# Kernel tuning notes

Measured on AMD Instinct MI355X. Metric: run time of the kernel, lower is better.

The kernel has to match this reference:

```python
import jax, jax.numpy as jnp
import numpy as np

B, N, C, H, AD, HID = 2, 1024, 768, 12, 8, 3072
SCALE = (C // H) ** -0.5


def setup_inputs() -> dict:
    key = jax.random.key(0)
    ks = jax.random.split(key, 32)
    inp = {}
    for i in range(5):
        inp[f"x{i}"] = jax.random.normal(ks[i], (B, N, C), jnp.float32)
    def w(i, shape, s=0.02):
        return jax.random.normal(ks[i], shape, jnp.float32) * s
    inp.update({
        "ln1_g": jnp.ones((C,), jnp.float32), "ln1_b": jnp.zeros((C,), jnp.float32),
        "ln2_g": jnp.ones((C,), jnp.float32), "ln2_b": jnp.zeros((C,), jnp.float32),
        "qkv_w": w(5, (C, 3 * C)), "qkv_b": jnp.zeros((3 * C,), jnp.float32),
        "proj_w": w(6, (C, C)), "proj_b": jnp.zeros((C,), jnp.float32),
        "fc1_w": w(7, (C, HID)), "fc1_b": jnp.zeros((HID,), jnp.float32),
        "fc2_w": w(8, (HID, C)), "fc2_b": jnp.zeros((C,), jnp.float32),
        "at_dw": w(9, (C, AD)), "at_db": jnp.zeros((AD,), jnp.float32),
        "at_mw": w(10, (AD, AD)), "at_mb": jnp.zeros((AD,), jnp.float32),
        "at_uw": w(11, (AD, C)), "at_ub": jnp.zeros((C,), jnp.float32),
        "a2_dw": w(12, (C, AD)), "a2_db": jnp.zeros((AD,), jnp.float32),
        "a2_mw": w(13, (AD, AD)), "a2_mb": jnp.zeros((AD,), jnp.float32),
        "a2_uw": w(14, (AD, C)), "a2_ub": jnp.zeros((C,), jnp.float32),
    })
    return inp


def _ln(x, g, b, eps=1e-5):
    mu = x.mean(-1, keepdims=True)
    xc = x - mu
    var = (xc * xc).mean(-1, keepdims=True)
    return xc * jax.lax.rsqrt(var + eps) * g + b


def _adapter(x, dw, db, mw, mb, uw, ub):
    h = x @ dw + db          # bottleneck down [., AD]
    h = h @ mw + mb          # mid
    return h @ uw + ub       # up back to C


def _attn(x, qkv_w, qkv_b, proj_w, proj_b):
    # x: [S, B, N, C] (streams folded in leading axis)
    s, b, n, c = x.shape
    qkv = (x @ qkv_w + qkv_b).reshape(s, b, n, 3, H, c // H)
    q, k, v = jnp.moveaxis(qkv, 3, 0)            # each [S,B,N,H,D]
    scores = jnp.einsum('sbnhd,sbmhd->sbhnm', q * SCALE, k)  # fp32; clamp is a no-op
    p = jax.nn.softmax(scores, axis=-1)
    o = jnp.einsum('sbhnm,sbmhd->sbnhd', p, v).reshape(s, b, n, c)
    return o @ proj_w + proj_b


def reference(x0, x1, x2, x3, x4,
              ln1_g, ln1_b, ln2_g, ln2_b,
              qkv_w, qkv_b, proj_w, proj_b,
              fc1_w, fc1_b, fc2_w, fc2_b,
              at_dw, at_db, at_mw, at_mb, at_uw, at_ub,
              a2_dw, a2_db, a2_mw, a2_mb, a2_uw, a2_ub):
    xs = jnp.stack([x0, x1, x2, x3, x4])          # [5,B,N,C]
    n1 = _ln(xs, ln1_g, ln1_b)
    a1 = _adapter(n1, at_dw, at_db, at_mw, at_mb, at_uw, at_ub)
    ao = _attn(n1, qkv_w, qkv_b, proj_w, proj_b)
    # cross-stream residuals: x01=a1[0], x12=a1[1], ..., x10=a1[1], x21=a1[2], ...
    y0 = xs[0] + ao[0] + a1[1]
    y1 = xs[1] + ao[1] + a1[0] + a1[2]
    y2 = xs[2] + ao[2] + a1[1] + a1[3]
    y3 = xs[3] + ao[3] + a1[2] + a1[4]
    y4 = xs[4] + ao[4] + a1[3]
    ys = jnp.stack([y0, y1, y2, y3, y4])
    a2 = _adapter(_ln(ys, ln1_g, ln1_b), a2_dw, a2_db, a2_mw, a2_mb, a2_uw, a2_ub)
    h = _ln(ys, ln2_g, ln2_b) @ fc1_w + fc1_b
    m = jax.nn.gelu(h, approximate=False) @ fc2_w + fc2_b
    z0 = ys[0] + m[0] + a2[1]
    z1 = ys[1] + m[1] + a2[0] + a2[2]
    z2 = ys[2] + m[2] + a2[1] + a2[3]
    z3 = ys[3] + m[3] + a2[2] + a2[4]
    z4 = ys[4] + m[4] + a2[3]
    return jnp.stack([z0, z1, z2, z3, z4])        # [5,B,N,C]
```

## Files before the change

kernel.cpp:

```cpp
#include <hip/hip_runtime.h>
#include <math.h>

typedef __bf16 bf16;
typedef __attribute__((ext_vector_type(8))) __bf16 bf16x8;
typedef __attribute__((ext_vector_type(4))) __bf16 bf16x4;
typedef __attribute__((ext_vector_type(4))) float f32x4;
typedef __attribute__((ext_vector_type(16))) float f32x16;

#define TOK   10240
#define CD    768
#define NQKV  2304
#define NHID  3072
#define SEQ   1024
#define NH    12

__device__ __forceinline__ f32x4 mfma16(bf16x8 a, bf16x8 b, f32x4 c) {
  return __builtin_amdgcn_mfma_f32_16x16x32_bf16(a, b, c, 0, 0, 0);
}
__device__ __forceinline__ f32x16 mfma32(bf16x8 a, bf16x8 b, f32x16 c) {
  return __builtin_amdgcn_mfma_f32_32x32x16_bf16(a, b, c, 0, 0, 0);
}

__device__ __forceinline__ void gload16(const void* g, void* l) {
  __builtin_amdgcn_global_load_lds(
      (const __attribute__((address_space(1))) void*)g,
      (__attribute__((address_space(3))) void*)l, 16, 0, 0);
}

__device__ __forceinline__ unsigned pack2(bf16 a, bf16 b) {
  union { unsigned short u[2]; unsigned v; } x;
  x.u[0] = __builtin_bit_cast(unsigned short, a);
  x.u[1] = __builtin_bit_cast(unsigned short, b);
  return x.v;
}

__device__ __forceinline__ f32x4 b4tof(const bf16* p) {
  bf16x4 v = *(const bf16x4*)p;
  f32x4 r;
#pragma unroll
  for (int j = 0; j < 4; ++j) r[j] = (float)v[j];
  return r;
}

__device__ __forceinline__ float fast_gelu(float v) {
  float u = 0.7978845608f * (v + 0.044715f * v * v * v);
  float e = __expf(fminf(2.f * u, 30.f));
  return 0.5f * v * (1.f + (e - 1.f) / (e + 1.f));
}

__global__ __launch_bounds__(256) void transpose_to_bf16(
    const float* __restrict__ in, bf16* __restrict__ out, int K, int N) {
  __shared__ float tile[32][33];
  const int bn = blockIdx.x * 32, bk = blockIdx.y * 32;
  const int r = threadIdx.x >> 5, c = threadIdx.x & 31;
#pragma unroll
  for (int i = 0; i < 4; ++i)
    tile[r + 8 * i][c] = in[(size_t)(bk + r + 8 * i) * N + bn + c];
  __syncthreads();
#pragma unroll
  for (int i = 0; i < 4; ++i)
    out[(size_t)(bn + r + 8 * i) * K + bk + c] = (bf16)tile[c][r + 8 * i];
}

__global__ __launch_bounds__(256) void ln5_kernel(
    const float* __restrict__ x0, const float* __restrict__ x1,
    const float* __restrict__ x2, const float* __restrict__ x3,
    const float* __restrict__ x4, const float* __restrict__ g,
    const float* __restrict__ b, bf16* __restrict__ out) {
  const int w = threadIdx.x >> 6, lane = threadIdx.x & 63;
  const int row = blockIdx.x * 4 + w;
  const int s = row >> 11, rem = row & 2047;
  const float* xp;
  switch (s) {
    case 0: xp = x0; break; case 1: xp = x1; break; case 2: xp = x2; break;
    case 3: xp = x3; break; default: xp = x4; break;
  }
  const f32x4* xr = (const f32x4*)(xp + (size_t)rem * CD);
  f32x4 v[3];
#pragma unroll
  for (int i = 0; i < 3; ++i) v[i] = xr[lane + 64 * i];
  float sum = 0.f;
#pragma unroll
  for (int i = 0; i < 3; ++i)
#pragma unroll
    for (int j = 0; j < 4; ++j) sum += v[i][j];
#pragma unroll
  for (int m = 32; m >= 1; m >>= 1) sum += __shfl_xor(sum, m);
  const float mu = sum * (1.f / 768.f);
  float vs = 0.f;
#pragma unroll
  for (int i = 0; i < 3; ++i)
#pragma unroll
    for (int j = 0; j < 4; ++j) { float d = v[i][j] - mu; vs += d * d; }
#pragma unroll
  for (int m = 32; m >= 1; m >>= 1) vs += __shfl_xor(vs, m);
  const float rstd = rsqrtf(vs * (1.f / 768.f) + 1e-5f);
  const f32x4* gp = (const f32x4*)g;
  const f32x4* bp = (const f32x4*)b;
  bf16* orow = out + (size_t)row * CD;
#pragma unroll
  for (int i = 0; i < 3; ++i) {
    const int c4 = lane + 64 * i;
    f32x4 gg = gp[c4], bb = bp[c4];
    bf16x4 o;
#pragma unroll
    for (int j = 0; j < 4; ++j)
      o[j] = (bf16)((v[i][j] - mu) * rstd * gg[j] + bb[j]);
    *(bf16x4*)(orow + c4 * 4) = o;
  }
}

__global__ __launch_bounds__(256) void fuse_res_ln(
    const float* __restrict__ x0, const float* __restrict__ x1,
    const float* __restrict__ x2, const float* __restrict__ x3,
    const float* __restrict__ x4, const bf16* __restrict__ m01,
    const bf16* __restrict__ a, float* __restrict__ ys,
    const float* __restrict__ g1, const float* __restrict__ b1,
    const float* __restrict__ g2, const float* __restrict__ b2,
    bf16* __restrict__ o1, bf16* __restrict__ o2) {
  const int w = threadIdx.x >> 6, lane = threadIdx.x & 63;
  const int row = blockIdx.x * 4 + w;
  const int s = row >> 11, rem = row & 2047;
  const float* xp;
  switch (s) {
    case 0: xp = x0; break; case 1: xp = x1; break; case 2: xp = x2; break;
    case 3: xp = x3; break; default: xp = x4; break;
  }
  const f32x4* xr = (const f32x4*)(xp + (size_t)rem * CD);
  const bf16* p0 = m01 + (size_t)row * CD;
  const bf16* p1 = m01 + (size_t)TOK * CD + (size_t)row * CD;
  const bf16* am = a + (size_t)(row - 2048) * CD;
  const bf16* ap = a + (size_t)(row + 2048) * CD;
  f32x4 v[3];
#pragma unroll
  for (int i = 0; i < 3; ++i) {
    const int c4 = lane + 64 * i;
    f32x4 t = xr[c4] + b4tof(p0 + c4 * 4) + b4tof(p1 + c4 * 4);
    if (s > 0) t += b4tof(am + c4 * 4);
    if (s < 4) t += b4tof(ap + c4 * 4);
    v[i] = t;
  }
  f32x4* yr = (f32x4*)(ys + (size_t)row * CD);
#pragma unroll
  for (int i = 0; i < 3; ++i) yr[lane + 64 * i] = v[i];

  float sum = 0.f;
#pragma unroll
  for (int i = 0; i < 3; ++i)
#pragma unroll
    for (int j = 0; j < 4; ++j) sum += v[i][j];
#pragma unroll
  for (int m = 32; m >= 1; m >>= 1) sum += __shfl_xor(sum, m);
  const float mu = sum * (1.f / 768.f);
  float vs = 0.f;
#pragma unroll
  for (int i = 0; i < 3; ++i)
#pragma unroll
    for (int j = 0; j < 4; ++j) { float d = v[i][j] - mu; vs += d * d; }
#pragma unroll
  for (int m = 32; m >= 1; m >>= 1) vs += __shfl_xor(vs, m);
  const float rstd = rsqrtf(vs * (1.f / 768.f) + 1e-5f);
  bf16* r1 = o1 + (size_t)row * CD;
  bf16* r2 = o2 + (size_t)row * CD;
#pragma unroll
  for (int i = 0; i < 3; ++i) {
    const int c4 = lane + 64 * i;
    f32x4 gg1 = ((const f32x4*)g1)[c4], bb1 = ((const f32x4*)b1)[c4];
    f32x4 gg2 = ((const f32x4*)g2)[c4], bb2 = ((const f32x4*)b2)[c4];
    bf16x4 oa, ob;
#pragma unroll
    for (int j = 0; j < 4; ++j) {
      float n = (v[i][j] - mu) * rstd;
      oa[j] = (bf16)(n * gg1[j] + bb1[j]);
      ob[j] = (bf16)(n * gg2[j] + bb2[j]);
    }
    *(bf16x4*)(r1 + c4 * 4) = oa;
    *(bf16x4*)(r2 + c4 * 4) = ob;
  }
}

template <int EPI>
__global__ __launch_bounds__(512, 2) void gemm256(
    const bf16* __restrict__ A, const bf16* __restrict__ Bt,
    const float* __restrict__ bias, void* __restrict__ Cout, int N, int Klen,
    int ldk, int nbn, int bpk, size_t kpstride) {
  __shared__ bf16 As[2][8192];
  __shared__ bf16 Bs[2][8192];
  const int t = threadIdx.x, lane = t & 63, w = t >> 6;
  const int wm = w >> 2, wn = w & 3;

  const int chunkg = gridDim.x >> 3;
  const int wg = (blockIdx.x & 7) * chunkg + (blockIdx.x >> 3);
  const int kp = wg / bpk, rem = wg % bpk;
  const int bm = rem / nbn, bn = rem % nbn;

  f32x4 acc[8][4] = {};

  const int srow = t >> 2;
  const int scol = ((t & 3) ^ ((srow >> 1) & 3)) << 3;
  const size_t koff = (size_t)kp * Klen;
  const bf16* Ab = A + (size_t)(bm * 256 + srow) * ldk + koff + scol;
  const bf16* Bb = Bt + (size_t)(bn * 256 + srow) * ldk + koff + scol;
  const size_t r128 = (size_t)128 * ldk;

  auto stage = [&](int buf, int kt) {
    const bf16* ga = Ab + (size_t)kt * 32;
    const bf16* gb = Bb + (size_t)kt * 32;
    gload16(ga, &As[buf][w * 512]);
    gload16(ga + r128, &As[buf][4096 + w * 512]);
    gload16(gb, &Bs[buf][w * 512]);
    gload16(gb + r128, &Bs[buf][4096 + w * 512]);
  };

  const int arow = wm * 128 + (lane & 15);
  const int brow = wn * 64 + (lane & 15);
  const int achn = (((lane >> 4) ^ ((lane >> 1) & 3)) << 3);

  stage(0, 0);
  stage(1, 1);
  asm volatile("s_waitcnt vmcnt(4)" ::: "memory");
  __builtin_amdgcn_s_barrier();

  const int NT = Klen >> 5;
  bf16x8 af[8], bfr[4];

  for (int kt = 0; kt < NT; ++kt) {
    const int buf = kt & 1;
#pragma unroll
    for (int m_ = 0; m_ < 8; ++m_)
      af[m_] = *(const bf16x8*)&As[buf][(arow + m_ * 16) * 32 + achn];
#pragma unroll
    for (int n_ = 0; n_ < 4; ++n_)
      bfr[n_] = *(const bf16x8*)&Bs[buf][(brow + n_ * 16) * 32 + achn];
    asm volatile("s_waitcnt lgkmcnt(0)" ::: "memory");
    __builtin_amdgcn_s_barrier();
    if (kt + 2 < NT) {
      stage(buf, kt + 2);
      asm volatile("s_waitcnt vmcnt(4)" ::: "memory");
    } else {
      asm volatile("s_waitcnt vmcnt(0)" ::: "memory");
    }
    __builtin_amdgcn_s_barrier();
    __builtin_amdgcn_s_setprio(1);
#pragma unroll
    for (int m_ = 0; m_ < 8; ++m_)
#pragma unroll
      for (int n_ = 0; n_ < 4; ++n_)
        acc[m_][n_] = mfma16(af[m_], bfr[n_], acc[m_][n_]);
    __builtin_amdgcn_s_setprio(0);
  }

#pragma unroll
  for (int m_ = 0; m_ < 8; ++m_) {
    const int grow0 = bm * 256 + wm * 128 + m_ * 16 + (lane >> 4) * 4;
#pragma unroll
    for (int n_ = 0; n_ < 4; ++n_) {
      const int gcol = bn * 256 + wn * 64 + n_ * 16 + (lane & 15);
      const float bv = (kp == 0) ? bias[gcol] : 0.f;
#pragma unroll
      for (int r = 0; r < 4; ++r) {
        float v = acc[m_][n_][r] + bv;
        if (EPI == 2) v = fast_gelu(v);
        const size_t idx = (size_t)(grow0 + r) * N + gcol + kp * kpstride;
        if (EPI == 0) ((float*)Cout)[idx] = v;
        else ((bf16*)Cout)[idx] = (bf16)v;
      }
    }
  }
}

__global__ __launch_bounds__(256, 3) void attn_v2(
    const bf16* __restrict__ qkv, bf16* __restrict__ obuf) {
  __shared__ bf16 Ks[2][4096];
  __shared__ bf16 Vt[2][4096];
  const int t = threadIdx.x, lane = t & 63, w = t >> 6;
  const int g = lane >> 5, q32 = lane & 31, rq7 = q32 & 7;

  const int xcd = blockIdx.x & 7, slot = blockIdx.x >> 3;
  const int work = xcd * 120 + slot;
  const int sbh = work >> 3, qt = work & 7;
  const int sb = sbh / NH, h = sbh % NH;
  const size_t tokbase = (size_t)sb * SEQ;
  const int qoff = h * 64, koff = CD + h * 64, voff = 2 * CD + h * 64;

  const int qrow = qt * 128 + w * 32 + q32;
  bf16x8 qf[4];
  {
    const bf16* qp = qkv + (tokbase + qrow) * NQKV + qoff + g * 8;
#pragma unroll
    for (int kd = 0; kd < 4; ++kd) {
      bf16x8 v = *(const bf16x8*)(qp + kd * 16);
#pragma unroll
      for (int j = 0; j < 8; ++j) v[j] = (bf16)((float)v[j] * 0.125f);
      qf[kd] = v;
    }
  }

  const int skv1 = t >> 3, sc1 = (t & 7) ^ (skv1 & 7);
  const int skv2 = (t + 256) >> 3, sc2 = (t & 7) ^ (skv2 & 7);
  const int vkv0 = 2 * (t & 31);
  const int vd0 = 8 * (t >> 5);
  const int c0 = (vkv0 & 51) | ((vkv0 & 4) << 1) | ((vkv0 & 8) >> 1);
  const int vchunk = c0 >> 3, vsub = c0 & 7;
  const bf16* kbase = qkv + tokbase * NQKV + koff;
  const bf16* vbase = qkv + tokbase * NQKV + voff;

  {
    const bf16* kb0 = kbase;
    gload16(kb0 + (size_t)skv1 * NQKV + sc1 * 8, &Ks[0][w * 512]);
    gload16(kb0 + (size_t)skv2 * NQKV + sc2 * 8, &Ks[0][2048 + w * 512]);
    const bf16* vp = vbase + (size_t)vkv0 * NQKV + vd0;
    bf16x8 r0 = *(const bf16x8*)vp;
    bf16x8 r1 = *(const bf16x8*)(vp + NQKV);
#pragma unroll
    for (int j = 0; j < 8; ++j) {
      const int d = vd0 + j;
      *(unsigned*)&Vt[0][d * 64 + ((vchunk ^ j) << 3) + vsub] =
          pack2(r0[j], r1[j]);
    }
  }
  __syncthreads();

  float m_run = -1e30f, l_run = 0.f;
  f32x16 oT0 = {}, oT1 = {};
  int cur = 0;

  for (int kt = 0; kt < 16; ++kt) {
    bf16x8 nv0, nv1;
    if (kt < 15) {
      const bf16* vp = vbase + (size_t)((kt + 1) * 64 + vkv0) * NQKV + vd0;
      nv0 = *(const bf16x8*)vp;
      nv1 = *(const bf16x8*)(vp + NQKV);
      const bf16* kb0 = kbase + (size_t)(kt + 1) * 64 * NQKV;
      gload16(kb0 + (size_t)skv1 * NQKV + sc1 * 8, &Ks[cur ^ 1][w * 512]);
      gload16(kb0 + (size_t)skv2 * NQKV + sc2 * 8,
              &Ks[cur ^ 1][2048 + w * 512]);
    }

    f32x16 sT0 = {}, sT1 = {};
#pragma unroll
    for (int kd = 0; kd < 4; ++kd) {
      bf16x8 kf0 =
          *(const bf16x8*)&Ks[cur][q32 * 64 + (((2 * kd + g) ^ rq7) << 3)];
      bf16x8 kf1 = *(const bf16x8*)&Ks[cur][(32 + q32) * 64 +
                                            (((2 * kd + g) ^ rq7) << 3)];
      sT0 = mfma32(kf0, qf[kd], sT0);
      sT1 = mfma32(kf1, qf[kd], sT1);
    }

    float mt = sT0[0];
#pragma unroll
    for (int r = 1; r < 16; ++r) mt = fmaxf(mt, sT0[r]);
#pragma unroll
    for (int r = 0; r < 16; ++r) mt = fmaxf(mt, sT1[r]);
    mt = fmaxf(mt, __shfl_xor(mt, 32));
    const float mnew = fmaxf(m_run, mt);
    const float alpha = __expf(m_run - mnew);
    m_run = mnew;
    float rs = 0.f;
#pragma unroll
    for (int r = 0; r < 16; ++r) {
      sT0[r] = __expf(sT0[r] - mnew);
      rs += sT0[r];
    }
#pragma unroll
    for (int r = 0; r < 16; ++r) {
      sT1[r] = __expf(sT1[r] - mnew);
      rs += sT1[r];
    }
    rs += __shfl_xor(rs, 32);
    l_run = l_run * alpha + rs;
#pragma unroll
    for (int r = 0; r < 16; ++r) { oT0[r] *= alpha; oT1[r] *= alpha; }

    bf16x8 pa[4];
#pragma unroll
    for (int hh = 0; hh < 2; ++hh)
#pragma unroll
      for (int j = 0; j < 8; ++j) {
        pa[hh][j] = (bf16)sT0[8 * hh + j];
        pa[2 + hh][j] = (bf16)sT1[8 * hh + j];
      }

#pragma unroll
    for (int ks = 0; ks < 4; ++ks) {
      bf16x8 vf0 =
          *(const bf16x8*)&Vt[cur][q32 * 64 + (((2 * ks + g) ^ rq7) << 3)];
      bf16x8 vf1 = *(const bf16x8*)&Vt[cur][(32 + q32) * 64 +
                                            (((2 * ks + g) ^ rq7) << 3)];
      oT0 = mfma32(vf0, pa[ks], oT0);
      oT1 = mfma32(vf1, pa[ks], oT1);
    }

    if (kt < 15) {
#pragma unroll
      for (int j = 0; j < 8; ++j) {
        const int d = vd0 + j;
        *(unsigned*)&Vt[cur ^ 1][d * 64 + ((vchunk ^ j) << 3) + vsub] =
            pack2(nv0[j], nv1[j]);
      }
    }
    __syncthreads();
    cur ^= 1;
  }

  const float rl = 1.f / l_run;
  bf16* orow = obuf + (tokbase + qrow) * CD + h * 64;
#pragma unroll
  for (int m = 0; m < 4; ++m) {
    bf16x4 o0, o1;
#pragma unroll
    for (int r = 0; r < 4; ++r) {
      o0[r] = (bf16)(oT0[4 * m + r] * rl);
      o1[r] = (bf16)(oT1[4 * m + r] * rl);
    }
    *(bf16x4*)(orow + 8 * m + 4 * g) = o0;
    *(bf16x4*)(orow + 32 + 8 * m + 4 * g) = o1;
  }
}

__global__ __launch_bounds__(256) void adapter_kernel(
    const bf16* __restrict__ X, const float* __restrict__ dw,
    const float* __restrict__ db, const float* __restrict__ mw,
    const float* __restrict__ mb, const float* __restrict__ uw,
    const float* __restrict__ ub, bf16* __restrict__ out) {
  const int tok = blockIdx.x * 4 + (threadIdx.x >> 6);
  const int lane = threadIdx.x & 63;
  const bf16* xr = X + (size_t)tok * CD;
  float xv[12];
#pragma unroll
  for (int i = 0; i < 12; ++i) xv[i] = (float)xr[lane + 64 * i];
  float h1[8] = {0, 0, 0, 0, 0, 0, 0, 0};
#pragma unroll
  for (int i = 0; i < 12; ++i) {
    const f32x4* dr = (const f32x4*)(dw + (size_t)(lane + 64 * i) * 8);
    f32x4 d0 = dr[0], d1 = dr[1];
#pragma unroll
    for (int j = 0; j < 4; ++j) {
      h1[j] += xv[i] * d0[j];
      h1[4 + j] += xv[i] * d1[j];
    }
  }
#pragma unroll
  for (int m = 1; m < 64; m <<= 1)
#pragma unroll
    for (int j = 0; j < 8; ++j) h1[j] += __shfl_xor(h1[j], m);
#pragma unroll
  for (int j = 0; j < 8; ++j) h1[j] += db[j];
  float h2[8];
#pragma unroll
  for (int k = 0; k < 8; ++k) {
    float v = mb[k];
#pragma unroll
    for (int j = 0; j < 8; ++j) v += h1[j] * mw[j * 8 + k];
    h2[k] = v;
  }
#pragma unroll
  for (int i = 0; i < 12; ++i) {
    const int c = lane + 64 * i;
    float v = ub[c];
#pragma unroll
    for (int k = 0; k < 8; ++k) v += h2[k] * uw[k * CD + c];
    out[(size_t)tok * CD + c] = (bf16)v;
  }
}

__global__ __launch_bounds__(256) void cross_residual(
    const float* __restrict__ ys, const bf16* __restrict__ m01,
    const bf16* __restrict__ a, float* __restrict__ out) {
  const int s = blockIdx.y;
  const size_t i = (size_t)blockIdx.x * 256 + threadIdx.x;
  const size_t spitch = (size_t)2048 * 768 / 4;
  const size_t sb = (size_t)s * spitch;
  const size_t mstride = (size_t)TOK * CD / 4;
  f32x4 v = ((const f32x4*)ys)[sb + i];
  v += b4tof(m01 + (sb + i) * 4);
  v += b4tof(m01 + (mstride + sb + i) * 4);
  if (s > 0) v += b4tof(a + (sb - spitch + i) * 4);
  if (s < 4) v += b4tof(a + (sb + spitch + i) * 4);
  ((f32x4*)out)[sb + i] = v;
}

#define OFF_WTQKV  ((size_t)0)
#define OFF_WTPROJ ((size_t)3538944)
#define OFF_WTFC1  ((size_t)4718592)
#define OFF_WTFC2  ((size_t)9437184)
#define OFF_N1     ((size_t)14155776)
#define OFF_BIG    ((size_t)29884416)
#define OFF_OBUF   ((size_t)77070336)
#define OFF_AOM    ((size_t)92798976)
#define OFF_A12    ((size_t)124256256)
#define OFF_YS     ((size_t)155713536)
#define OFF_L2Y    ((size_t)187170816)

extern "C" void kernel_launch(void* const* d_in, const int* in_sizes, int n_in,
                              void* d_out, int out_size, void* d_ws,
                              size_t ws_size, hipStream_t stream) {
  const float* x0 = (const float*)d_in[0];
  const float* x1 = (const float*)d_in[1];
  const float* x2 = (const float*)d_in[2];
  const float* x3 = (const float*)d_in[3];
  const float* x4 = (const float*)d_in[4];
  const float* ln1_g = (const float*)d_in[5];
  const float* ln1_b = (const float*)d_in[6];
  const float* ln2_g = (const float*)d_in[7];
  const float* ln2_b = (const float*)d_in[8];
  const float* qkv_w = (const float*)d_in[9];
  const float* qkv_b = (const float*)d_in[10];
  const float* proj_w = (const float*)d_in[11];
  const float* proj_b = (const float*)d_in[12];
  const float* fc1_w = (const float*)d_in[13];
  const float* fc1_b = (const float*)d_in[14];
  const float* fc2_w = (const float*)d_in[15];
  const float* fc2_b = (const float*)d_in[16];
  const float* at_dw = (const float*)d_in[17];
  const float* at_db = (const float*)d_in[18];
  const float* at_mw = (const float*)d_in[19];
  const float* at_mb = (const float*)d_in[20];
  const float* at_uw = (const float*)d_in[21];
  const float* at_ub = (const float*)d_in[22];
  const float* a2_dw = (const float*)d_in[23];
  const float* a2_db = (const float*)d_in[24];
  const float* a2_mw = (const float*)d_in[25];
  const float* a2_mb = (const float*)d_in[26];
  const float* a2_uw = (const float*)d_in[27];
  const float* a2_ub = (const float*)d_in[28];

  char* ws = (char*)d_ws;
  bf16* wt_qkv = (bf16*)(ws + OFF_WTQKV);
  bf16* wt_proj = (bf16*)(ws + OFF_WTPROJ);
  bf16* wt_fc1 = (bf16*)(ws + OFF_WTFC1);
  bf16* wt_fc2 = (bf16*)(ws + OFF_WTFC2);
  bf16* n1 = (bf16*)(ws + OFF_N1);
  bf16* qkvb = (bf16*)(ws + OFF_BIG);
  bf16* obuf = (bf16*)(ws + OFF_OBUF);
  bf16* mbuf = (bf16*)(ws + OFF_AOM);
  bf16* a12 = (bf16*)(ws + OFF_A12);
  float* ysb = (float*)(ws + OFF_YS);
  bf16* l2y = (bf16*)(ws + OFF_L2Y);

  const dim3 b256(256);
  const dim3 b512(512);

  transpose_to_bf16<<<dim3(72, 24), b256, 0, stream>>>(qkv_w, wt_qkv, 768, 2304);
  transpose_to_bf16<<<dim3(24, 24), b256, 0, stream>>>(proj_w, wt_proj, 768, 768);
  transpose_to_bf16<<<dim3(96, 24), b256, 0, stream>>>(fc1_w, wt_fc1, 768, 3072);
  transpose_to_bf16<<<dim3(24, 96), b256, 0, stream>>>(fc2_w, wt_fc2, 3072, 768);

  ln5_kernel<<<2560, b256, 0, stream>>>(x0, x1, x2, x3, x4, ln1_g, ln1_b, n1);

  gemm256<1><<<360, b512, 0, stream>>>(n1, wt_qkv, qkv_b, qkvb, NQKV, 768, 768,
                                       9, 360, 0);

  adapter_kernel<<<2560, b256, 0, stream>>>(n1, at_dw, at_db, at_mw, at_mb,
                                            at_uw, at_ub, a12);

  attn_v2<<<960, b256, 0, stream>>>(qkvb, obuf);

  gemm256<1><<<240, b512, 0, stream>>>(obuf, wt_proj, proj_b, mbuf, CD, 384,
                                       768, 3, 120, (size_t)TOK * CD);

  fuse_res_ln<<<2560, b256, 0, stream>>>(x0, x1, x2, x3, x4, mbuf, a12, ysb,
                                         ln1_g, ln1_b, ln2_g, ln2_b, n1, l2y);

  adapter_kernel<<<2560, b256, 0, stream>>>(n1, a2_dw, a2_db, a2_mw, a2_mb,
                                            a2_uw, a2_ub, a12);

  gemm256<2><<<480, b512, 0, stream>>>(l2y, wt_fc1, fc1_b, qkvb, NHID, 768,
                                       768, 12, 480, 0);

  gemm256<1><<<240, b512, 0, stream>>>(qkvb, wt_fc2, fc2_b, mbuf, CD, 1536,
                                       3072, 3, 120, (size_t)TOK * CD);

  cross_residual<<<dim3(1536, 5), b256, 0, stream>>>(ysb, mbuf, a12,
                                                     (float*)d_out);
}
```

Measured before the change: 389.2 us.

## Restructure GEMM to 4 waves with 128x128 warp tiles and triple buffering

The 256x256 GEMM tile kernel now runs 256 threads (4 waves) instead of 512, so each wave computes a 128x128 sub-tile with an 8x8 MFMA accumulator grid. The shared-memory pipeline moves from double to triple buffering. The prefetch for stage kt+2 is issued before the MFMA block and waited on after it, which removes the second barrier per iteration. This raises register pressure (256 accumulator floats per lane) and LDS use, and launch bounds drop to one block per SIMD group, cutting occupancy in exchange for more reuse per wave and better load/compute overlap.

```diff
diff --git a/kernel.cpp b/kernel.cpp
--- a/kernel.cpp
+++ b/kernel.cpp
@@ -180,82 +180,84 @@
 }
 
 template <int EPI>
-__global__ __launch_bounds__(512, 2) void gemm256(
+__global__ __launch_bounds__(256, 1) void gemm256(
     const bf16* __restrict__ A, const bf16* __restrict__ Bt,
     const float* __restrict__ bias, void* __restrict__ Cout, int N, int Klen,
     int ldk, int nbn, int bpk, size_t kpstride) {
-  __shared__ bf16 As[2][8192];
-  __shared__ bf16 Bs[2][8192];
+  __shared__ bf16 As[3][8192];
+  __shared__ bf16 Bs[3][8192];
   const int t = threadIdx.x, lane = t & 63, w = t >> 6;
-  const int wm = w >> 2, wn = w & 3;
+  const int wm = w >> 1, wn = w & 1;
 
   const int chunkg = gridDim.x >> 3;
   const int wg = (blockIdx.x & 7) * chunkg + (blockIdx.x >> 3);
   const int kp = wg / bpk, rem = wg % bpk;
   const int bm = rem / nbn, bn = rem % nbn;
 
-  f32x4 acc[8][4] = {};
+  f32x4 acc[8][8] = {};
 
   const int srow = t >> 2;
   const int scol = ((t & 3) ^ ((srow >> 1) & 3)) << 3;
   const size_t koff = (size_t)kp * Klen;
   const bf16* Ab = A + (size_t)(bm * 256 + srow) * ldk + koff + scol;
   const bf16* Bb = Bt + (size_t)(bn * 256 + srow) * ldk + koff + scol;
-  const size_t r128 = (size_t)128 * ldk;
+  const size_t r64 = (size_t)64 * ldk;
 
   auto stage = [&](int buf, int kt) {
     const bf16* ga = Ab + (size_t)kt * 32;
     const bf16* gb = Bb + (size_t)kt * 32;
-    gload16(ga, &As[buf][w * 512]);
-    gload16(ga + r128, &As[buf][4096 + w * 512]);
-    gload16(gb, &Bs[buf][w * 512]);
-    gload16(gb + r128, &Bs[buf][4096 + w * 512]);
+#pragma unroll
+    for (int i = 0; i < 4; ++i)
+      gload16(ga + i * r64, &As[buf][i * 2048 + w * 512]);
+#pragma unroll
+    for (int i = 0; i < 4; ++i)
+      gload16(gb + i * r64, &Bs[buf][i * 2048 + w * 512]);
   };
 
   const int arow = wm * 128 + (lane & 15);
-  const int brow = wn * 64 + (lane & 15);
+  const int brow = wn * 128 + (lane & 15);
   const int achn = (((lane >> 4) ^ ((lane >> 1) & 3)) << 3);
 
   stage(0, 0);
   stage(1, 1);
-  asm volatile("s_waitcnt vmcnt(4)" ::: "memory");
+  asm volatile("s_waitcnt vmcnt(8)" ::: "memory");
   __builtin_amdgcn_s_barrier();
 
   const int NT = Klen >> 5;
-  bf16x8 af[8], bfr[4];
+  bf16x8 af[8], bfr[8];
+  int buf = 0;
 
   for (int kt = 0; kt < NT; ++kt) {
-    const int buf = kt & 1;
 #pragma unroll
     for (int m_ = 0; m_ < 8; ++m_)
       af[m_] = *(const bf16x8*)&As[buf][(arow + m_ * 16) * 32 + achn];
 #pragma unroll
-    for (int n_ = 0; n_ < 4; ++n_)
+    for (int n_ = 0; n_ < 8; ++n_)
       bfr[n_] = *(const bf16x8*)&Bs[buf][(brow + n_ * 16) * 32 + achn];
     asm volatile("s_waitcnt lgkmcnt(0)" ::: "memory");
     __builtin_amdgcn_s_barrier();
-    if (kt + 2 < NT) {
-      stage(buf, kt + 2);
-      asm volatile("s_waitcnt vmcnt(4)" ::: "memory");
-    } else {
-      asm volatile("s_waitcnt vmcnt(0)" ::: "memory");
-    }
-    __builtin_amdgcn_s_barrier();
+    const int nbuf = (buf + 2 >= 3) ? buf - 1 : buf + 2;
+    if (kt + 2 < NT) stage(nbuf, kt + 2);
     __builtin_amdgcn_s_setprio(1);
 #pragma unroll
     for (int m_ = 0; m_ < 8; ++m_)
 #pragma unroll
-      for (int n_ = 0; n_ < 4; ++n_)
+      for (int n_ = 0; n_ < 8; ++n_)
         acc[m_][n_] = mfma16(af[m_], bfr[n_], acc[m_][n_]);
     __builtin_amdgcn_s_setprio(0);
+    if (kt + 2 < NT)
+      asm volatile("s_waitcnt vmcnt(8)" ::: "memory");
+    else
+      asm volatile("s_waitcnt vmcnt(0)" ::: "memory");
+    buf = (buf + 1 >= 3) ? 0 : buf + 1;
   }
 
 #pragma unroll
   for (int m_ = 0; m_ < 8; ++m_) {
     const int grow0 = bm * 256 + wm * 128 + m_ * 16 + (lane >> 4) * 4;
 #pragma unroll
-    for (int n_ = 0; n_ < 4; ++n_) {
-      const int gcol = bn * 256 + wn * 64 + n_ * 16 + (lane & 15);
+    for (int n_ = 0; n_ < 8; ++n_) {
+      const int gcol = bn * 256 + wn * 128 + n_ * 16 + (lane & 15);
       const float bv = (kp == 0) ? bias[gcol] : 0.f;
 #pragma unroll
       for (int r = 0; r < 4; ++r) {
@@ -540,7 +542,6 @@
   bf16* l2y = (bf16*)(ws + OFF_L2Y);
 
   const dim3 b256(256);
-  const dim3 b512(512);
 
   transpose_to_bf16<<<dim3(72, 24), b256, 0, stream>>>(qkv_w, wt_qkv, 768, 2304);
   transpose_to_bf16<<<dim3(24, 24), b256, 0, stream>>>(proj_w, wt_proj, 768, 768);
@@ -549,7 +550,7 @@
 
   ln5_kernel<<<2560, b256, 0, stream>>>(x0, x1, x2, x3, x4, ln1_g, ln1_b, n1);
 
-  gemm256<1><<<360, b512, 0, stream>>>(n1, wt_qkv, qkv_b, qkvb, NQKV, 768, 768,
+  gemm256<1><<<360, b256, 0, stream>>>(n1, wt_qkv, qkv_b, qkvb, NQKV, 768, 768,
                                        9, 360, 0);
 
   adapter_kernel<<<2560, b256, 0, stream>>>(n1, at_dw, at_db, at_mw, at_mb,
@@ -557,7 +558,7 @@
 
   attn_v2<<<960, b256, 0, stream>>>(qkvb, obuf);
 
-  gemm256<1><<<240, b512, 0, stream>>>(obuf, wt_proj, proj_b, mbuf, CD, 384,
+  gemm256<1><<<240, b256, 0, stream>>>(obuf, wt_proj, proj_b, mbuf, CD, 384,
                                        768, 3, 120, (size_t)TOK * CD);
 
   fuse_res_ln<<<2560, b256, 0, stream>>>(x0, x1, x2, x3, x4, mbuf, a12, ysb,
@@ -566,10 +567,10 @@
   adapter_kernel<<<2560, b256, 0, stream>>>(n1, a2_dw, a2_db, a2_mw, a2_mb,
                                             a2_uw, a2_ub, a12);
 
-  gemm256<2><<<480, b512, 0, stream>>>(l2y, wt_fc1, fc1_b, qkvb, NHID, 768,
+  gemm256<2><<<480, b256, 0, stream>>>(l2y, wt_fc1, fc1_b, qkvb, NHID, 768,
                                        768, 12, 480, 0);
 
-  gemm256<1><<<240, b512, 0, stream>>>(qkvb, wt_fc2, fc2_b, mbuf, CD, 1536,
+  gemm256<1><<<240, b256, 0, stream>>>(qkvb, wt_fc2, fc2_b, mbuf, CD, 1536,
                                        3072, 3, 120, (size_t)TOK * CD);
 
   cross_residual<<<dim3(1536, 5), b256, 0, stream>>>(ysb, mbuf, a12,
```

Measured after the change: 435.8 us. 1.12x slower.
